# Kernel optimization log

Hardware: AMD Instinct MI355X
Metric: run time of the kernel (lower is better)

Reference implementation:

```python
import jax, jax.numpy as jnp
import numpy as np


def setup_inputs() -> dict:
    key = jax.random.key(0)
    k1, k2 = jax.random.split(key)
    n = 16384
    y = jax.random.normal(k1, (n,), dtype=jnp.float32)          # sign = event indicator, |y| = time
    y_hat = jax.random.normal(k2, (n, 1), dtype=jnp.float32)    # risk scores
    return {"y": y, "y_hat": y_hat}


def reference(y, y_hat):
    T = jnp.abs(y)                       # [n] observed times
    E = (y > 0).astype(jnp.float32)      # [n] event indicator (1 = uncensored)
    theta = y_hat.reshape(-1)            # [n]
    # Risk set: R[i, j] = 1 if T[j] >= T[i]
    R = (T[None, :] >= T[:, None]).astype(theta.dtype)  # [n, n]
    risk_sum = jnp.sum(jnp.exp(theta)[None, :] * R, axis=1)     # [n]
    loss = -jnp.mean((theta - jnp.log(risk_sum)) * E)
    return loss
```

## Files before the change

### kernel.cpp

```cpp
#include <hip/hip_runtime.h>


constexpr int   B     = 4096;
constexpr int   C     = 64;
constexpr float SCALE = 512.0f;
constexpr int   BPT   = B / 256;

__global__ __launch_bounds__(256) void k_zero(int* zbase, int nwords)
{
    const int i = blockIdx.x * 256 + threadIdx.x;
    if (i < nwords) zbase[i] = 0;
}

__global__ __launch_bounds__(256) void k_fill(
    const float* __restrict__ y, const float* __restrict__ yhat,
    int* __restrict__ cnt, float* __restrict__ bw, float2* __restrict__ padded)
{
    const int i = blockIdx.x * 256 + threadIdx.x;
    const float T = fabsf(y[i]);
    const float w = expf(yhat[i]);
    int b = (int)(T * SCALE);
    b = (b > B - 1) ? (B - 1) : b;
    atomicAdd(&bw[b], w);
    const int pos = atomicAdd(&cnt[b], 1);
    if (pos < C) padded[b * C + pos] = make_float2(T, w);
}

__global__ __launch_bounds__(256) void k_main(
    const float* __restrict__ y, const float* __restrict__ yhat,
    const int* __restrict__ cnt, const float* __restrict__ bw,
    const float2* __restrict__ padded, float* __restrict__ acc,
    int* __restrict__ done, float* __restrict__ out, int n)
{
    __shared__ float sbw[B];
    __shared__ float sred[4];

    const int tid = threadIdx.x;
    const int i   = blockIdx.x * 256 + tid;
    const int lane = tid & 63, wid = tid >> 6;

    for (int j = tid; j < B; j += 256) sbw[j] = bw[j];

    const float yi    = y[i];
    const float theta = yhat[i];
    const float T     = fabsf(yi);
    int b = (int)(T * SCALE);
    b = (b > B - 1) ? (B - 1) : b;
    __syncthreads();

    const int c0 = tid * BPT;
    float s = 0.0f;
#pragma unroll
    for (int k = 0; k < BPT; ++k) s += sbw[c0 + k];

    float x = s;
#pragma unroll
    for (int off = 1; off < 64; off <<= 1) {
        const float t = __shfl_down(x, off, 64);
        if (lane + off < 64) x += t;
    }
    if (lane == 0) sred[wid] = x;
    __syncthreads();
    float above = 0.0f;
    for (int w2 = wid + 1; w2 < 4; ++w2) above += sred[w2];
    __syncthreads();

    float run = above + (x - s);
#pragma unroll
    for (int k = BPT - 1; k >= 0; --k) {
        const float v = sbw[c0 + k];
        sbw[c0 + k] = run;
        run += v;
    }
    __syncthreads();

    float rs = sbw[b];
    int c = cnt[b];
    c = (c > C) ? C : c;
    const float2* base = padded + (size_t)b * C;
    for (int j = 0; j < c; ++j) {
        const float2 o = base[j];
        rs += (o.x >= T) ? o.y : 0.0f;
    }

    float p = (yi > 0.0f) ? (theta - logf(rs)) : 0.0f;
#pragma unroll
    for (int off = 32; off > 0; off >>= 1) p += __shfl_down(p, off, 64);
    if (lane == 0) sred[wid] = p;
    __syncthreads();
    if (tid == 0) {
        const float bs = sred[0] + sred[1] + sred[2] + sred[3];
        atomicAdd(acc, bs);
        __threadfence();
        const int old = atomicAdd(done, 1);
        if (old == (int)gridDim.x - 1) {
            const float tot = atomicAdd(acc, 0.0f);
            out[0] = -tot / (float)n;
        }
    }
}

extern "C" void kernel_launch(void* const* d_in, const int* in_sizes, int n_in,
                              void* d_out, int out_size, void* d_ws, size_t ws_size,
                              hipStream_t stream) {
    const float* y    = (const float*)d_in[0];
    const float* yhat = (const float*)d_in[1];
    float* out        = (float*)d_out;
    const int n       = in_sizes[0];

    char* p = (char*)d_ws;
    int*    cnt    = (int*)p;      p += (size_t)B * sizeof(int);
    float*  bw     = (float*)p;    p += (size_t)B * sizeof(float);
    float*  acc    = (float*)p;    p += sizeof(float);
    int*    done   = (int*)p;      p += sizeof(int);
    float2* padded = (float2*)p;

    const int zwords = 2 * B + 2;
    k_zero<<<dim3((zwords + 255) / 256), dim3(256), 0, stream>>>((int*)d_ws, zwords);
    k_fill<<<dim3(n / 256), dim3(256), 0, stream>>>(y, yhat, cnt, bw, padded);
    k_main<<<dim3(n / 256), dim3(256), 0, stream>>>(y, yhat, cnt, bw, padded,
                                                    acc, done, out, n);
}
```

Baseline: 28.10 us.

## Replace per-block full suffix scan with two-level coarse/fine bucket sums

Each block of the main kernel no longer loads all 4096 bucket weights into shared memory and runs a block-wide suffix scan. The fill kernel now also builds 64 coarse-chunk weights, reducing in shared memory before doing global atomics. Each thread sums the coarse chunks above its chunk plus the fine buckets above its bucket within the chunk, using float4 loads, and reads the padded entries as pairs. The aim is to remove the 16KB shared-memory staging and the multiple barriers, at the cost of 128 redundant loads per thread, which should mostly hit in cache.

```diff
diff --git a/kernel.cpp b/kernel.cpp
--- a/kernel.cpp
+++ b/kernel.cpp
@@ -4,7 +4,6 @@
 constexpr int   B     = 4096;
 constexpr int   C     = 64;
 constexpr float SCALE = 512.0f;
-constexpr int   BPT   = B / 256;
 
 __global__ __launch_bounds__(256) void k_zero(int* zbase, int nwords)
 {
@@ -14,78 +13,94 @@
 
 __global__ __launch_bounds__(256) void k_fill(
     const float* __restrict__ y, const float* __restrict__ yhat,
-    int* __restrict__ cnt, float* __restrict__ bw, float2* __restrict__ padded)
+    int* __restrict__ cnt, float* __restrict__ fineBW,
+    float* __restrict__ coarseW, float2* __restrict__ padded)
 {
-    const int i = blockIdx.x * 256 + threadIdx.x;
+    __shared__ float scw[64];
+    const int tid = threadIdx.x;
+    const int i   = blockIdx.x * 256 + tid;
+
+    if (tid < 64) scw[tid] = 0.0f;
+    __syncthreads();
+
     const float T = fabsf(y[i]);
     const float w = expf(yhat[i]);
     int b = (int)(T * SCALE);
     b = (b > B - 1) ? (B - 1) : b;
-    atomicAdd(&bw[b], w);
+
+    atomicAdd(&fineBW[b], w);
+    atomicAdd(&scw[b >> 6], w);
     const int pos = atomicAdd(&cnt[b], 1);
     if (pos < C) padded[b * C + pos] = make_float2(T, w);
+
+    __syncthreads();
+    if (tid < 64 && scw[tid] != 0.0f) atomicAdd(&coarseW[tid], scw[tid]);
 }
 
 __global__ __launch_bounds__(256) void k_main(
     const float* __restrict__ y, const float* __restrict__ yhat,
-    const int* __restrict__ cnt, const float* __restrict__ bw,
-    const float2* __restrict__ padded, float* __restrict__ acc,
-    int* __restrict__ done, float* __restrict__ out, int n)
+    const int* __restrict__ cnt, const float* __restrict__ fineBW,
+    const float* __restrict__ coarseW, const float2* __restrict__ padded,
+    float* __restrict__ acc, int* __restrict__ done,
+    float* __restrict__ out, int n)
 {
-    __shared__ float sbw[B];
-    __shared__ float sred[4];
-
     const int tid = threadIdx.x;
     const int i   = blockIdx.x * 256 + tid;
     const int lane = tid & 63, wid = tid >> 6;
-
-    for (int j = tid; j < B; j += 256) sbw[j] = bw[j];
 
     const float yi    = y[i];
     const float theta = yhat[i];
     const float T     = fabsf(yi);
     int b = (int)(T * SCALE);
     b = (b > B - 1) ? (B - 1) : b;
-    __syncthreads();
+    const int ch = b >> 6;
+    const int bl = b & 63;
 
-    const int c0 = tid * BPT;
-    float s = 0.0f;
-#pragma unroll
-    for (int k = 0; k < BPT; ++k) s += sbw[c0 + k];
-
-    float x = s;
-#pragma unroll
-    for (int off = 1; off < 64; off <<= 1) {
-        const float t = __shfl_down(x, off, 64);
-        if (lane + off < 64) x += t;
-    }
-    if (lane == 0) sred[wid] = x;
-    __syncthreads();
-    float above = 0.0f;
-    for (int w2 = wid + 1; w2 < 4; ++w2) above += sred[w2];
-    __syncthreads();
-
-    float run = above + (x - s);
-#pragma unroll
-    for (int k = BPT - 1; k >= 0; --k) {
-        const float v = sbw[c0 + k];
-        sbw[c0 + k] = run;
-        run += v;
-    }
-    __syncthreads();
-
-    float rs = sbw[b];
     int c = cnt[b];
     c = (c > C) ? C : c;
-    const float2* base = padded + (size_t)b * C;
-    for (int j = 0; j < c; ++j) {
-        const float2 o = base[j];
-        rs += (o.x >= T) ? o.y : 0.0f;
+
+    float rs = 0.0f;
+
+    const float4* cw4 = (const float4*)coarseW;
+#pragma unroll
+    for (int q = 0; q < 16; ++q) {
+        const float4 v = cw4[q];
+        const int j0 = q * 4;
+        rs += ((j0 + 0) > ch ? v.x : 0.0f);
+        rs += ((j0 + 1) > ch ? v.y : 0.0f);
+        rs += ((j0 + 2) > ch ? v.z : 0.0f);
+        rs += ((j0 + 3) > ch ? v.w : 0.0f);
+    }
+
+    const float4* fw4 = (const float4*)(fineBW + (ch << 6));
+#pragma unroll
+    for (int q = 0; q < 16; ++q) {
+        const float4 v = fw4[q];
+        const int j0 = q * 4;
+        rs += ((j0 + 0) > bl ? v.x : 0.0f);
+        rs += ((j0 + 1) > bl ? v.y : 0.0f);
+        rs += ((j0 + 2) > bl ? v.z : 0.0f);
+        rs += ((j0 + 3) > bl ? v.w : 0.0f);
+    }
+
+    const float4* base4 = (const float4*)(padded + (size_t)b * C);
+    const int pairs = c >> 1;
+    for (int q = 0; q < pairs; ++q) {
+        const float4 e = base4[q];
+        rs += (e.x >= T ? e.y : 0.0f);
+        rs += (e.z >= T ? e.w : 0.0f);
+    }
+    if (c & 1) {
+        const float2 o = padded[(size_t)b * C + (c - 1)];
+        rs += (o.x >= T ? o.y : 0.0f);
     }
 
     float p = (yi > 0.0f) ? (theta - logf(rs)) : 0.0f;
+
 #pragma unroll
     for (int off = 32; off > 0; off >>= 1) p += __shfl_down(p, off, 64);
+
+    __shared__ float sred[4];
     if (lane == 0) sred[wid] = p;
     __syncthreads();
     if (tid == 0) {
@@ -109,15 +124,18 @@
     const int n       = in_sizes[0];
 
     char* p = (char*)d_ws;
-    int*    cnt    = (int*)p;      p += (size_t)B * sizeof(int);
-    float*  bw     = (float*)p;    p += (size_t)B * sizeof(float);
-    float*  acc    = (float*)p;    p += sizeof(float);
-    int*    done   = (int*)p;      p += sizeof(int);
-    float2* padded = (float2*)p;
+    float2* padded  = (float2*)p;  p += (size_t)B * C * sizeof(float2);
+    int*    zbase   = (int*)p;
+    int*    cnt     = (int*)p;     p += (size_t)B * sizeof(int);
+    float*  fineBW  = (float*)p;   p += (size_t)B * sizeof(float);
+    float*  coarseW = (float*)p;   p += 64 * sizeof(float);
+    float*  acc     = (float*)p;   p += sizeof(float);
+    int*    done    = (int*)p;
 
-    const int zwords = 2 * B + 2;
-    k_zero<<<dim3((zwords + 255) / 256), dim3(256), 0, stream>>>((int*)d_ws, zwords);
-    k_fill<<<dim3(n / 256), dim3(256), 0, stream>>>(y, yhat, cnt, bw, padded);
-    k_main<<<dim3(n / 256), dim3(256), 0, stream>>>(y, yhat, cnt, bw, padded,
-                                                    acc, done, out, n);
+    const int zwords = B + B + 64 + 2;
+    k_zero<<<dim3((zwords + 255) / 256), dim3(256), 0, stream>>>(zbase, zwords);
+    k_fill<<<dim3(n / 256), dim3(256), 0, stream>>>(y, yhat, cnt, fineBW,
+                                                    coarseW, padded);
+    k_main<<<dim3(n / 256), dim3(256), 0, stream>>>(y, yhat, cnt, fineBW, coarseW,
+                                                    padded, acc, done, out, n);
 }
```

Result: faster. 25.87 us, median of 2 (-7.9%).
